# Performance work log

Measured on AMD Instinct MI355X. Metric: run time of the kernel, lower is better.

The kernel has to match this reference:

```python
import jax, jax.numpy as jnp
import numpy as np

N_NODES = 50000
N_EDGES = 1600000
NUM_GRAPHS = 512
NEG_SLOPE = 0.2


def _glorot(key, shape):
    fan_in, fan_out = shape[0], shape[-1]
    lim = jnp.sqrt(6.0 / (fan_in + fan_out))
    return jax.random.uniform(key, shape, jnp.float32, -lim, lim)


def setup_inputs() -> dict:
    key = jax.random.key(0)
    ks = jax.random.split(key, 10)
    x = jax.random.normal(ks[0], (N_NODES, 133), jnp.float32)
    edge_index = jax.random.randint(ks[1], (2, N_EDGES), 0, N_NODES, jnp.int64)
    batch = jnp.sort(jax.random.randint(ks[2], (N_NODES,), 0, NUM_GRAPHS, jnp.int64))
    # conv1: GATConv(133 -> 8, heads=8, concat=True)
    W1 = _glorot(ks[3], (133, 64))
    att_src1 = _glorot(ks[4], (8, 8))   # [H, C]
    att_dst1 = _glorot(ks[5], (8, 8))
    b1 = jnp.zeros((64,), jnp.float32)
    # conv2: GATConv(64 -> 2, heads=1, concat=True)
    W2 = _glorot(ks[6], (64, 2))
    att_src2 = _glorot(ks[7], (1, 2))
    att_dst2 = _glorot(ks[8], (1, 2))
    b2 = jnp.zeros((2,), jnp.float32)
    return {"x": x, "edge_index": edge_index, "batch": batch,
            "W1": W1, "att_src1": att_src1, "att_dst1": att_dst1, "b1": b1,
            "W2": W2, "att_src2": att_src2, "att_dst2": att_dst2, "b2": b2}


def gat_conv(x, src, dst, W, att_src, att_dst, bias):
    """PyG GATConv (add_self_loops already applied via src/dst), concat=True, eval mode."""
    N = x.shape[0]
    H, C = att_src.shape
    h = (x @ W).reshape(N, H, C)                      # [N, H, C]
    a_src = jnp.sum(h * att_src[None], axis=-1)       # [N, H]
    a_dst = jnp.sum(h * att_dst[None], axis=-1)       # [N, H]
    e = a_src[src] + a_dst[dst]                       # [E, H]
    e = jnp.where(e > 0, e, NEG_SLOPE * e)            # leaky_relu
    # segment softmax over incoming edges of each dst node
    e_max = jax.ops.segment_max(e, dst, num_segments=N)  # [N, H]
    e_exp = jnp.exp(e - e_max[dst])
    denom = jax.ops.segment_sum(e_exp, dst, num_segments=N)
    alpha = e_exp / jnp.maximum(denom, 1e-16)[dst]    # [E, H]
    msg = h[src] * alpha[:, :, None]                  # [E, H, C]
    out = jax.ops.segment_sum(msg, dst, num_segments=N)  # [N, H, C]
    return out.reshape(N, H * C) + bias


def reference(x, edge_index, batch, W1, att_src1, att_dst1, b1, W2, att_src2, att_dst2, b2):
    N = x.shape[0]
    loops = jnp.arange(N, dtype=edge_index.dtype)
    src = jnp.concatenate([edge_index[0], loops])
    dst = jnp.concatenate([edge_index[1], loops])
    # dropout layers are identity in eval mode
    h = gat_conv(x, src, dst, W1, att_src1, att_dst1, b1)   # [N, 64]
    h = jax.nn.elu(h)
    h = gat_conv(h, src, dst, W2, att_src2, att_dst2, b2)   # [N, 2]
    out = jax.ops.segment_sum(h, batch, num_segments=NUM_GRAPHS)  # [G, 2]
    return out
```

## Files before the change

### kernel.cpp

```cpp
#include <hip/hip_runtime.h>
#include <hip/hip_fp16.h>

#define NN 50000
#define NE 1600000
#define NG 512
#define NEG 0.2f

#define NBKT 782
#define CHUNK 4096
#define NSB ((NE + CHUNK - 1) / CHUNK)
#define CAP 3072
#define NSLOT 32

typedef _Float16 half8 __attribute__((ext_vector_type(8)));
typedef float f32x4 __attribute__((ext_vector_type(4)));


__global__ __launch_bounds__(256) void k_init(const float* __restrict__ W1,
                                              _Float16* __restrict__ W1f,
                                              int* __restrict__ bcursor,
                                              float* __restrict__ out) {
    int i = blockIdx.x * 256 + threadIdx.x;
    if (i < 1280) {
        int f = i >> 6, l = i & 63;
        int kt = f >> 2, ct = f & 3;
        int g = l >> 4, c16 = l & 15;
#pragma unroll
        for (int j = 0; j < 8; ++j) {
            int k = kt * 32 + g * 8 + j;
            float v = (k < 133) ? W1[k * 64 + ct * 16 + c16] : 0.f;
            W1f[i * 8 + j] = (_Float16)v;
        }
    } else if (i < 1280 + NBKT * 16) {
        bcursor[i - 1280] = 0;
    } else if (i < 1280 + NBKT * 16 + NG * 2) {
        out[i - 1280 - NBKT * 16] = 0.f;
    }
}

__global__ __launch_bounds__(256) void k_linmfma(const float* __restrict__ x,
                                                 const _Float16* __restrict__ W1f,
                                                 const float* __restrict__ attS,
                                                 const float* __restrict__ attD,
                                                 __half* __restrict__ h1h,
                                                 float* __restrict__ aS,
                                                 float* __restrict__ aD) {
    const int wid = (blockIdx.x * 256 + threadIdx.x) >> 6;
    const int nb  = wid * 16;
    if (nb >= NN) return;
    const int l   = threadIdx.x & 63;
    const int g   = l >> 4, c16 = l & 15;
    const long xbase = (long)(nb + c16) * 133;

    half8 bfr[5][4];
#pragma unroll
    for (int kt = 0; kt < 5; ++kt)
#pragma unroll
        for (int ct = 0; ct < 4; ++ct)
            bfr[kt][ct] = *reinterpret_cast<const half8*>(W1f + ((kt * 4 + ct) * 64 + l) * 8);

    f32x4 acc[4] = {{0.f,0.f,0.f,0.f},{0.f,0.f,0.f,0.f},{0.f,0.f,0.f,0.f},{0.f,0.f,0.f,0.f}};
#pragma unroll
    for (int kt = 0; kt < 5; ++kt) {
        half8 a;
#pragma unroll
        for (int i = 0; i < 8; ++i) {
            int k = kt * 32 + g * 8 + i;
            a[i] = (_Float16)((k < 133) ? x[xbase + k] : 0.f);
        }
#pragma unroll
        for (int ct = 0; ct < 4; ++ct)
            acc[ct] = __builtin_amdgcn_mfma_f32_16x16x32_f16(a, bfr[kt][ct], acc[ct], 0, 0, 0);
    }

#pragma unroll
    for (int ct = 0; ct < 4; ++ct) {
        const int col  = ct * 16 + c16;
        const int head = col >> 3;
        const float as_w = attS[head * 8 + (col & 7)];
        const float ad_w = attD[head * 8 + (col & 7)];
#pragma unroll
        for (int r = 0; r < 4; ++r) {
            const int n = nb + g * 4 + r;
            float v = acc[ct][r];
            h1h[n * 64 + col] = __float2half(v);
            float ps = v * as_w, pd = v * ad_w;
            ps += __shfl_xor(ps, 1, 64); pd += __shfl_xor(pd, 1, 64);
            ps += __shfl_xor(ps, 2, 64); pd += __shfl_xor(pd, 2, 64);
            ps += __shfl_xor(ps, 4, 64); pd += __shfl_xor(pd, 4, 64);
            if ((l & 7) == 0) {
                aS[n * 8 + head] = ps;
                aD[n * 8 + head] = pd;
            }
        }
    }
}

__global__ __launch_bounds__(256) void k_binscatter(const int* __restrict__ ei,
                                                    int* __restrict__ bcursor,
                                                    unsigned* __restrict__ binned) {
    __shared__ int hist[NBKT];
    __shared__ int basel[NBKT];
    const int t = threadIdx.x;
    const int estart = blockIdx.x * CHUNK;
    const int eend = min(estart + CHUNK, NE);

    for (int i = t; i < NBKT; i += 256) hist[i] = 0;
    __syncthreads();
    for (int e = estart + t; e < eend; e += 256)
        atomicAdd(&hist[ei[NE + e] >> 6], 1);
    __syncthreads();
    for (int i = t; i < NBKT; i += 256) {
        int h = hist[i];
        basel[i] = h ? (i * CAP + atomicAdd(&bcursor[i * 16], h)) : 0;
    }
    __syncthreads();
    for (int i = t; i < NBKT; i += 256) hist[i] = 0;
    __syncthreads();
    for (int e = estart + t; e < eend; e += 256) {
        int s = ei[e];
        int d = ei[NE + e];
        int b = d >> 6;
        int r = atomicAdd(&hist[b], 1);
        int pos = basel[b] + r;
        if (pos < (b + 1) * CAP) binned[pos] = ((unsigned)s << 6) | (unsigned)(d & 63);
    }
}

__global__ __launch_bounds__(256) void k_buildcsr(const unsigned* __restrict__ binned,
                                                  const int* __restrict__ bcursor,
                                                  int2* __restrict__ row_se,
                                                  unsigned short* __restrict__ csr) {
    __shared__ unsigned edg[CAP];
    __shared__ unsigned short csrl[CAP];
    __shared__ int deg[64], scn[64], cur[64];

    const int b = blockIdx.x, t = threadIdx.x;
    const int ebase = b * CAP;
    const int ecnt  = min(bcursor[b * 16], CAP);
    const int nbase = b << 6;
    const int ncnt  = min(64, NN - nbase);

    for (int i = t; i < ecnt; i += 256) edg[i] = binned[ebase + i];
    if (t < 64) deg[t] = 0;
    __syncthreads();
    for (int i = t; i < ecnt; i += 256) atomicAdd(&deg[edg[i] & 63], 1);
    __syncthreads();
    if (t < 64) scn[t] = deg[t];
    __syncthreads();
    for (int o = 1; o < 64; o <<= 1) {
        int v = (t < 64 && t >= o) ? scn[t - o] : 0;
        __syncthreads();
        if (t < 64) scn[t] += v;
        __syncthreads();
    }
    if (t < 64) {
        cur[t] = scn[t] - deg[t];
        if (t < ncnt) row_se[nbase + t] = make_int2(ebase + scn[t] - deg[t], ebase + scn[t]);
    }
    __syncthreads();
    for (int i = t; i < ecnt; i += 256) {
        unsigned pk = edg[i];
        int pos = atomicAdd(&cur[pk & 63], 1);
        csrl[pos] = (unsigned short)(pk >> 6);
    }
    __syncthreads();
    for (int i = t; i < ecnt; i += 256) csr[ebase + i] = csrl[i];
}

__global__ __launch_bounds__(256) void k_gather1(const unsigned short* __restrict__ csr,
                                                 const int2* __restrict__ row_se,
                                                 const float* __restrict__ aS,
                                                 const float* __restrict__ aD,
                                                 const unsigned* __restrict__ h1u,
                                                 const float* __restrict__ b1,
                                                 const float* __restrict__ W2,
                                                 const float* __restrict__ attS2,
                                                 const float* __restrict__ attD2,
                                                 float4* __restrict__ node4) {
    __shared__ float exs[4][64 * 8];
    __shared__ int   svs[4][64];

    const int sub  = threadIdx.x >> 6;
    const int lane = threadIdx.x & 63;
    const int n    = (blockIdx.x * 256 + threadIdx.x) >> 6;
    const int hp   = lane & 7;
    const int ebl  = lane >> 3;
    const int half = lane >> 5;
    const int c    = lane & 31;
    const int hc   = c >> 2;

    const float aDhp = aD[n * 8 + hp];
    const int2 se = row_se[n];
    const int e0 = se.x, e1 = se.y;

    float2 acc = make_float2(0.f, 0.f);
    float den = 0.f;
    for (int base = e0; base < e1; base += 64) {
        const int cnt = min(64, e1 - base);
        int sv = (base + lane < e1) ? (int)csr[base + lane] : n;
        svs[sub][lane] = sv;

#pragma unroll
        for (int p = 0; p < 8; ++p) {
            int eb = p * 8 + ebl;
            int s  = svs[sub][eb];
            float ev = aS[s * 8 + hp] + aDhp;
            ev = fmaxf(ev, NEG * ev);
            float ex = __expf(ev);
            if (eb >= cnt) ex = 0.f;
            exs[sub][eb * 8 + hp] = ex;
            den += ex;
        }

        const int cnt8 = (cnt + 7) & ~7;
        for (int eb = 0; eb < cnt8; eb += 8) {
#pragma unroll
            for (int k = 0; k < 8; k += 2) {
                int   e2 = eb + k + half;
                int   s  = svs[sub][e2];
                float ex = exs[sub][e2 * 8 + hc];
                unsigned hv = h1u[s * 32 + c];
                float2 f2 = __half22float2(*reinterpret_cast<__half2*>(&hv));
                acc.x = fmaf(ex, f2.x, acc.x);
                acc.y = fmaf(ex, f2.y, acc.y);
            }
        }
    }
    den += __shfl_xor(den, 8, 64);
    den += __shfl_xor(den, 16, 64);
    den += __shfl_xor(den, 32, 64);
    float ev_s = aS[n * 8 + hp] + aDhp;
    ev_s = fmaxf(ev_s, NEG * ev_s);
    float ex_self = __expf(ev_s);
    den += ex_self;

    acc.x += __shfl_xor(acc.x, 32, 64);
    acc.y += __shfl_xor(acc.y, 32, 64);

    float den_c = __shfl(den, hc, 64);
    float ex_sc = __shfl(ex_self, hc, 64);

    unsigned hvs = h1u[n * 32 + c];
    float2 fs = __half22float2(*reinterpret_cast<__half2*>(&hvs));
    float inv = 1.f / fmaxf(den_c, 1e-16f);
    float2 bb = reinterpret_cast<const float2*>(b1)[c];
    float vx = fmaf(ex_sc, fs.x, acc.x) * inv + bb.x;
    float vy = fmaf(ex_sc, fs.y, acc.y) * inv + bb.y;
    vx = vx > 0.f ? vx : (__expf(vx) - 1.f);
    vy = vy > 0.f ? vy : (__expf(vy) - 1.f);

    float4 w = reinterpret_cast<const float4*>(W2)[c];
    float p0 = vx * w.x + vy * w.z;
    float p1 = vx * w.y + vy * w.w;
    p0 += __shfl_xor(p0, 1, 64);  p1 += __shfl_xor(p1, 1, 64);
    p0 += __shfl_xor(p0, 2, 64);  p1 += __shfl_xor(p1, 2, 64);
    p0 += __shfl_xor(p0, 4, 64);  p1 += __shfl_xor(p1, 4, 64);
    p0 += __shfl_xor(p0, 8, 64);  p1 += __shfl_xor(p1, 8, 64);
    p0 += __shfl_xor(p0, 16, 64); p1 += __shfl_xor(p1, 16, 64);
    if (lane == 0) {
        float s2 = p0 * attS2[0] + p1 * attS2[1];
        float d2 = p0 * attD2[0] + p1 * attD2[1];
        node4[n] = make_float4(p0, p1, s2, d2);
    }
}

__global__ __launch_bounds__(256) void k_gather2(const unsigned short* __restrict__ csr,
                                                 const int2* __restrict__ row_se,
                                                 const float4* __restrict__ node4,
                                                 const int* __restrict__ batch,
                                                 const float* __restrict__ b2,
                                                 float* __restrict__ out) {
    __shared__ float pool[NSLOT][2];
    __shared__ int gbase_s;
    const int t = threadIdx.x;
    const int n = blockIdx.x * 256 + t;

    if (t == 0) gbase_s = batch[blockIdx.x * 256];
    for (int i = t; i < NSLOT * 2; i += 256) (&pool[0][0])[i] = 0.f;
    __syncthreads();

    if (n < NN) {
        const float4 vn = node4[n];
        const float aDd = vn.w;

        float ev = vn.z + aDd;
        ev = fmaxf(ev, NEG * ev);
        float ex = __expf(ev);
        float den = ex, p0 = ex * vn.x, p1 = ex * vn.y;

        const int2 se = row_se[n];
#pragma unroll 4
        for (int e = se.x; e < se.y; ++e) {
            int s = csr[e];
            float4 vs = node4[s];
            float ev2 = vs.z + aDd;
            ev2 = fmaxf(ev2, NEG * ev2);
            float ex2 = __expf(ev2);
            den += ex2;
            p0 = fmaf(ex2, vs.x, p0);
            p1 = fmaf(ex2, vs.y, p1);
        }
        float inv = 1.f / fmaxf(den, 1e-16f);
        float v0 = p0 * inv + b2[0];
        float v1 = p1 * inv + b2[1];

        int g = batch[n];
        int slot = g - gbase_s;
        if (slot < NSLOT) {
            atomicAdd(&pool[slot][0], v0);
            atomicAdd(&pool[slot][1], v1);
        } else {
            atomicAdd(&out[g * 2 + 0], v0);
            atomicAdd(&out[g * 2 + 1], v1);
        }
    }
    __syncthreads();
    for (int i = t; i < NSLOT; i += 256) {
        float v0 = pool[i][0], v1 = pool[i][1];
        if (v0 != 0.f || v1 != 0.f) {
            int g = gbase_s + i;
            atomicAdd(&out[g * 2 + 0], v0);
            atomicAdd(&out[g * 2 + 1], v1);
        }
    }
}

extern "C" void kernel_launch(void* const* d_in, const int* in_sizes, int n_in,
                              void* d_out, int out_size, void* d_ws, size_t ws_size,
                              hipStream_t stream) {
    const float* x     = (const float*)d_in[0];
    const int*   ei    = (const int*)d_in[1];
    const int*   batch = (const int*)d_in[2];
    const float* W1    = (const float*)d_in[3];
    const float* attS1 = (const float*)d_in[4];
    const float* attD1 = (const float*)d_in[5];
    const float* b1    = (const float*)d_in[6];
    const float* W2    = (const float*)d_in[7];
    const float* attS2 = (const float*)d_in[8];
    const float* attD2 = (const float*)d_in[9];
    const float* b2    = (const float*)d_in[10];
    float* out = (float*)d_out;

    int* ws = (int*)d_ws;
    __half* h1h = (__half*)ws;
    unsigned* h1u = (unsigned*)ws;
    float* aS1 = (float*)(ws + (size_t)NN * 32);
    float* aD1 = (float*)(ws + (size_t)NN * 40);
    float4* node4 = (float4*)(ws + (size_t)NN * 48);
    int2* row_se  = (int2*)(ws + (size_t)NN * 52);
    int* bcursor  = ws + (size_t)NN * 54;
    _Float16* W1f = (_Float16*)(ws + (size_t)NN * 54 + 12544);
    unsigned* binned    = (unsigned*)(ws + (size_t)NN * 55);
    unsigned short* csr = (unsigned short*)(ws + (size_t)NN * 55 + (size_t)NBKT * CAP);

    k_init<<<(1280 + NBKT * 16 + NG * 2 + 255) / 256, 256, 0, stream>>>(W1, W1f, bcursor, out);
    k_linmfma<<<(NN / 16 + 3) / 4, 256, 0, stream>>>(x, W1f, attS1, attD1, h1h, aS1, aD1);
    k_binscatter<<<NSB, 256, 0, stream>>>(ei, bcursor, binned);
    k_buildcsr<<<NBKT, 256, 0, stream>>>(binned, bcursor, row_se, csr);
    k_gather1<<<NN / 4, 256, 0, stream>>>(csr, row_se, aS1, aD1, h1u, b1, W2,
                                          attS2, attD2, node4);
    k_gather2<<<(NN + 255) / 256, 256, 0, stream>>>(csr, row_se, node4, batch, b2, out);
}
```

Before: 118.9 us.

## Replace atomic bucket cursors with count/scan/place three-pass binning

Splits the single bin-scatter kernel into a per-chunk histogram kernel, a per-bucket exclusive scan across chunks, and a placement kernel. This removes global atomics on bucket cursors, and the zeroing of those cursors in init, and makes bucket offsets deterministic. The cost is two extra kernel launches, a second read of the destination indices, and the cnt/base arrays written to and read from global memory. Chunks become 512 blocks of 3125 edges each, which divides the edge count exactly.

```diff
diff --git a/kernel.cpp b/kernel.cpp
--- a/kernel.cpp
+++ b/kernel.cpp
@@ -7,8 +7,8 @@
 #define NEG 0.2f
 
 #define NBKT 782
-#define CHUNK 4096
-#define NSB ((NE + CHUNK - 1) / CHUNK)
+#define NSB 512
+#define CHUNK 3125
 #define CAP 3072
 #define NSLOT 32
 
@@ -18,7 +18,6 @@
 
 __global__ __launch_bounds__(256) void k_init(const float* __restrict__ W1,
                                               _Float16* __restrict__ W1f,
-                                              int* __restrict__ bcursor,
                                               float* __restrict__ out) {
     int i = blockIdx.x * 256 + threadIdx.x;
     if (i < 1280) {
@@ -31,10 +30,8 @@
             float v = (k < 133) ? W1[k * 64 + ct * 16 + c16] : 0.f;
             W1f[i * 8 + j] = (_Float16)v;
         }
-    } else if (i < 1280 + NBKT * 16) {
-        bcursor[i - 1280] = 0;
-    } else if (i < 1280 + NBKT * 16 + NG * 2) {
-        out[i - 1280 - NBKT * 16] = 0.f;
+    } else if (i < 1280 + NG * 2) {
+        out[i - 1280] = 0.f;
     }
 }
 
@@ -96,39 +93,61 @@
     }
 }
 
-__global__ __launch_bounds__(256) void k_binscatter(const int* __restrict__ ei,
-                                                    int* __restrict__ bcursor,
-                                                    unsigned* __restrict__ binned) {
+__global__ __launch_bounds__(256) void k_count(const int* __restrict__ ei,
+                                               int* __restrict__ cnt) {
+    __shared__ int hist[NBKT];
+    const int t = threadIdx.x, blk = blockIdx.x;
+    for (int i = t; i < NBKT; i += 256) hist[i] = 0;
+    __syncthreads();
+    const int estart = blk * CHUNK;
+    for (int e = estart + t; e < estart + CHUNK; e += 256)
+        atomicAdd(&hist[ei[NE + e] >> 6], 1);
+    __syncthreads();
+    for (int i = t; i < NBKT; i += 256) cnt[blk * NBKT + i] = hist[i];
+}
+
+__global__ __launch_bounds__(512) void k_scan(const int* __restrict__ cnt,
+                                              int* __restrict__ base,
+                                              int* __restrict__ tot) {
+    __shared__ int s[NSB];
+    const int b = blockIdx.x, t = threadIdx.x;
+    int v = cnt[t * NBKT + b];
+    s[t] = v;
+    __syncthreads();
+    for (int o = 1; o < NSB; o <<= 1) {
+        int u = (t >= o) ? s[t - o] : 0;
+        __syncthreads();
+        s[t] += u;
+        __syncthreads();
+    }
+    base[t * NBKT + b] = s[t] - v;
+    if (t == NSB - 1) tot[b] = s[t];
+}
+
+__global__ __launch_bounds__(256) void k_place(const int* __restrict__ ei,
+                                               const int* __restrict__ base,
+                                               unsigned* __restrict__ binned) {
     __shared__ int hist[NBKT];
     __shared__ int basel[NBKT];
-    const int t = threadIdx.x;
-    const int estart = blockIdx.x * CHUNK;
-    const int eend = min(estart + CHUNK, NE);
-
-    for (int i = t; i < NBKT; i += 256) hist[i] = 0;
-    __syncthreads();
-    for (int e = estart + t; e < eend; e += 256)
-        atomicAdd(&hist[ei[NE + e] >> 6], 1);
-    __syncthreads();
+    const int t = threadIdx.x, blk = blockIdx.x;
     for (int i = t; i < NBKT; i += 256) {
-        int h = hist[i];
-        basel[i] = h ? (i * CAP + atomicAdd(&bcursor[i * 16], h)) : 0;
-    }
-    __syncthreads();
-    for (int i = t; i < NBKT; i += 256) hist[i] = 0;
-    __syncthreads();
-    for (int e = estart + t; e < eend; e += 256) {
+        hist[i]  = 0;
+        basel[i] = base[blk * NBKT + i];
+    }
+    __syncthreads();
+    const int estart = blk * CHUNK;
+    for (int e = estart + t; e < estart + CHUNK; e += 256) {
         int s = ei[e];
         int d = ei[NE + e];
         int b = d >> 6;
         int r = atomicAdd(&hist[b], 1);
         int pos = basel[b] + r;
-        if (pos < (b + 1) * CAP) binned[pos] = ((unsigned)s << 6) | (unsigned)(d & 63);
+        if (pos < CAP) binned[b * CAP + pos] = ((unsigned)s << 6) | (unsigned)(d & 63);
     }
 }
 
 __global__ __launch_bounds__(256) void k_buildcsr(const unsigned* __restrict__ binned,
-                                                  const int* __restrict__ bcursor,
+                                                  const int* __restrict__ tot,
                                                   int2* __restrict__ row_se,
                                                   unsigned short* __restrict__ csr) {
     __shared__ unsigned edg[CAP];
@@ -137,7 +156,7 @@
 
     const int b = blockIdx.x, t = threadIdx.x;
     const int ebase = b * CAP;
-    const int ecnt  = min(bcursor[b * 16], CAP);
+    const int ecnt  = min(tot[b], CAP);
     const int nbase = b << 6;
     const int ncnt  = min(64, NN - nbase);
 
@@ -349,15 +368,19 @@
     float* aD1 = (float*)(ws + (size_t)NN * 40);
     float4* node4 = (float4*)(ws + (size_t)NN * 48);
     int2* row_se  = (int2*)(ws + (size_t)NN * 52);
-    int* bcursor  = ws + (size_t)NN * 54;
-    _Float16* W1f = (_Float16*)(ws + (size_t)NN * 54 + 12544);
-    unsigned* binned    = (unsigned*)(ws + (size_t)NN * 55);
-    unsigned short* csr = (unsigned short*)(ws + (size_t)NN * 55 + (size_t)NBKT * CAP);
-
-    k_init<<<(1280 + NBKT * 16 + NG * 2 + 255) / 256, 256, 0, stream>>>(W1, W1f, bcursor, out);
+    int* tot      = ws + (size_t)NN * 54;
+    _Float16* W1f = (_Float16*)(ws + (size_t)NN * 54 + 1024);
+    int* cnt      = ws + (size_t)NN * 55;
+    int* base     = ws + (size_t)NN * 55 + (size_t)NSB * NBKT;
+    unsigned* binned    = (unsigned*)(ws + (size_t)NN * 55 + 2 * (size_t)NSB * NBKT);
+    unsigned short* csr = (unsigned short*)(binned + (size_t)NBKT * CAP);
+
+    k_init<<<(1280 + NG * 2 + 255) / 256, 256, 0, stream>>>(W1, W1f, out);
     k_linmfma<<<(NN / 16 + 3) / 4, 256, 0, stream>>>(x, W1f, attS1, attD1, h1h, aS1, aD1);
-    k_binscatter<<<NSB, 256, 0, stream>>>(ei, bcursor, binned);
-    k_buildcsr<<<NBKT, 256, 0, stream>>>(binned, bcursor, row_se, csr);
+    k_count<<<NSB, 256, 0, stream>>>(ei, cnt);
+    k_scan<<<NBKT, NSB, 0, stream>>>(cnt, base, tot);
+    k_place<<<NSB, 256, 0, stream>>>(ei, base, binned);
+    k_buildcsr<<<NBKT, 256, 0, stream>>>(binned, tot, row_se, csr);
     k_gather1<<<NN / 4, 256, 0, stream>>>(csr, row_se, aS1, aD1, h1u, b1, W2,
                                           attS2, attD2, node4);
     k_gather2<<<(NN + 255) / 256, 256, 0, stream>>>(csr, row_se, node4, batch, b2, out);
```

Result: faster. 114.0 us (-4.1%).
